# Kernel optimization log

Hardware: AMD Instinct MI355X
Metric: run time of the kernel (lower is better)

Reference implementation:

```python
import jax, jax.numpy as jnp
import numpy as np

N = 50000          # nodes
E = 800000         # edges per metapath
P = 4              # metapaths
IN = 256           # in_size
D = 32 * 8         # out_size * layer_num_heads = 256
SEM_H = 128        # SemanticAttention hidden


def setup_inputs() -> dict:
    key = jax.random.key(0)
    ks = jax.random.split(key, 8)
    h = jax.random.normal(ks[0], (N, IN), dtype=jnp.float32)
    src = jax.random.randint(ks[1], (P, E), 0, N, dtype=jnp.int32)
    dst = jax.random.randint(ks[2], (P, E), 0, N, dtype=jnp.int32)
    # per-metapath GraphConv weights (Glorot-ish scale)
    W_gc = jax.random.normal(ks[3], (P, IN, D), dtype=jnp.float32) / np.sqrt(IN)
    b_gc = jnp.zeros((P, D), dtype=jnp.float32)
    # SemanticAttention: Linear(D, SEM_H) -> tanh -> Linear(SEM_H, 1, bias=False)
    W1 = jax.random.normal(ks[4], (D, SEM_H), dtype=jnp.float32) / np.sqrt(D)
    b1 = jnp.zeros((SEM_H,), dtype=jnp.float32)
    w2 = jax.random.normal(ks[5], (SEM_H,), dtype=jnp.float32) / np.sqrt(SEM_H)
    return {"h": h, "src": src, "dst": dst, "W_gc": W_gc, "b_gc": b_gc,
            "W1": W1, "b1": b1, "w2": w2}


def _graph_conv(h, src, dst, W, b):
    # DGL GraphConv with norm='both': D_dst^{-1/2} A D_src^{-1/2} (h W) + b
    ones = jnp.ones((src.shape[0],), dtype=h.dtype)
    deg_out = jnp.clip(jax.ops.segment_sum(ones, src, num_segments=N), 1.0)
    deg_in = jnp.clip(jax.ops.segment_sum(ones, dst, num_segments=N), 1.0)
    x = (h @ W) * jax.lax.rsqrt(deg_out)[:, None]          # [N, D]
    agg = jax.ops.segment_sum(x[src], dst, num_segments=N)  # gather-scatter [N, D]
    return agg * jax.lax.rsqrt(deg_in)[:, None] + b


def reference(h, src, dst, W_gc, b_gc, W1, b1, w2):
    # per-metapath GraphConv (fixed small loop over P metapaths)
    zs = [_graph_conv(h, src[p], dst[p], W_gc[p], b_gc[p]) for p in range(P)]
    z = jnp.stack(zs, axis=1)                               # [N, P, D]
    # SemanticAttention: project -> mean over nodes -> softmax over metapaths
    s = jnp.tanh(z @ W1 + b1) @ w2                          # [N, P]
    beta = jax.nn.softmax(s.mean(axis=0), axis=0)           # [P]
    return jnp.einsum('npd,p->nd', z, beta)                 # [N, D]
```

## Files before the change

### kernel.cpp

```cpp
#include <hip/hip_runtime.h>

#define NN 50000
#define NE 800000
#define NP 4
#define DIN 256
#define DD 256
#define NH 128
#define SA 40
#define NSEG 16
#define SEGE (NE / NSEG)
#define FCH 8192
#define NFC 7
#define SPAD(k) ((k) + ((k) >> 5))

typedef __attribute__((ext_vector_type(8))) short bf16x8;
typedef __attribute__((ext_vector_type(4))) float f32x4;

__device__ __forceinline__ unsigned short f2bf(float f) {
  unsigned u = __float_as_uint(f);
  u += 0x7fff + ((u >> 16) & 1);
  return (unsigned short)(u >> 16);
}
__device__ __forceinline__ float bfl(unsigned u) { return __uint_as_float(u << 16); }
__device__ __forceinline__ float bfh(unsigned u) { return __uint_as_float(u & 0xffff0000u); }


__global__ __launch_bounds__(256) void hist2d_kernel(const int* __restrict__ idx,
                                                     int* __restrict__ cnt) {
  int bx = blockIdx.x;
  int c = bx % NFC, s = bx / NFC;
  int p = blockIdx.y;
  int base = c * FCH, nk = min(FCH, NN - base);
  __shared__ int hs[FCH];
  for (int k = threadIdx.x; k < FCH; k += 256) hs[k] = 0;
  __syncthreads();
  const int4* a4 = (const int4*)(idx + (size_t)p * NE + (size_t)s * SEGE);
  for (int i = threadIdx.x; i < SEGE / 4; i += 256) {
    int4 v = a4[i];
    int k;
    k = v.x - base; if ((unsigned)k < (unsigned)nk) atomicAdd(&hs[k], 1);
    k = v.y - base; if ((unsigned)k < (unsigned)nk) atomicAdd(&hs[k], 1);
    k = v.z - base; if ((unsigned)k < (unsigned)nk) atomicAdd(&hs[k], 1);
    k = v.w - base; if ((unsigned)k < (unsigned)nk) atomicAdd(&hs[k], 1);
  }
  __syncthreads();
  int* out = cnt + (size_t)(p * NSEG + s) * NN + base;
  for (int k = threadIdx.x; k < nk; k += 256) out[k] = hs[k];
}


__global__ __launch_bounds__(1024) void scanA_kernel(
    int* __restrict__ cntD, const int* __restrict__ cntS,
    float* __restrict__ rin, float* __restrict__ rout,
    int* __restrict__ row_ptr, int* __restrict__ chunkdeg) {
  int c = blockIdx.x, p = blockIdx.y;
  int base = c * FCH, nk = min(FCH, NN - base);
  __shared__ int sdeg[FCH + (FCH >> 5)];
  __shared__ int wtot[16], wexc[16];
  int t = threadIdx.x;
  for (int kk = t; kk < FCH; kk += 1024) {
    int run = 0;
    if (kk < nk) {
      size_t o = (size_t)(p * NSEG) * NN + base + kk;
      for (int s = 0; s < NSEG; ++s) {
        size_t oo = o + (size_t)s * NN;
        int v = cntD[oo];
        cntD[oo] = run;
        run += v;
      }
      rin[(size_t)p * NN + base + kk] = rsqrtf((float)max(run, 1));
      int rs = 0;
      for (int s = 0; s < NSEG; ++s) rs += cntS[o + (size_t)s * NN];
      rout[(size_t)p * NN + base + kk] = rsqrtf((float)max(rs, 1));
    }
    sdeg[SPAD(kk)] = run;
  }
  __syncthreads();
  int loc[8];
  int ssum = 0;
#pragma unroll
  for (int j = 0; j < 8; ++j) { loc[j] = ssum; ssum += sdeg[SPAD(t * 8 + j)]; }
  int incl = ssum;
  int lane = t & 63, w = t >> 6;
#pragma unroll
  for (int o = 1; o < 64; o <<= 1) {
    int v = __shfl_up(incl, o);
    if (lane >= o) incl += v;
  }
  if (lane == 63) wtot[w] = incl;
  __syncthreads();
  if (t == 0) {
    int r = 0;
    for (int i = 0; i < 16; ++i) { wexc[i] = r; r += wtot[i]; }
  }
  __syncthreads();
  int tbase = wexc[w] + incl - ssum;
  int* rp = row_ptr + (size_t)p * (NN + 1) + base;
#pragma unroll
  for (int j = 0; j < 8; ++j) {
    int k = t * 8 + j;
    if (k < nk) rp[k] = tbase + loc[j];
  }
  if (t == 1023) chunkdeg[p * NFC + c] = tbase + ssum;
}


__global__ void scanB_kernel(const int* __restrict__ chunkdeg, int* __restrict__ chunk_base,
                             int* __restrict__ row_ptr) {
  int t = threadIdx.x;
  if (t < NP) {
    int run = 0;
    for (int c = 0; c < NFC; ++c) { chunk_base[t * NFC + c] = run; run += chunkdeg[t * NFC + c]; }
    row_ptr[(size_t)t * (NN + 1) + NN] = NE;
  }
}

__global__ __launch_bounds__(1024) void rpfin_kernel(int* __restrict__ row_ptr,
                                                     const int* __restrict__ chunk_base) {
  int k = blockIdx.x * 1024 + threadIdx.x, p = blockIdx.y;
  if (k < NN) row_ptr[(size_t)p * (NN + 1) + k] += chunk_base[p * NFC + (k >> 13)];
}


__global__ __launch_bounds__(256) void scatter_kernel(
    const int* __restrict__ src, const int* __restrict__ dst,
    const int* __restrict__ cntD, const int* __restrict__ row_ptr, int* __restrict__ col) {
  int bx = blockIdx.x;
  int c = bx % NFC, s = bx / NFC;
  int p = blockIdx.y;
  int base = c * FCH, nk = min(FCH, NN - base);
  __shared__ int cur[FCH];
  for (int k = threadIdx.x; k < nk; k += 256)
    cur[k] = row_ptr[(size_t)p * (NN + 1) + base + k] +
             cntD[(size_t)(p * NSEG + s) * NN + base + k];
  __syncthreads();
  const int4* d4 = (const int4*)(dst + (size_t)p * NE + (size_t)s * SEGE);
  const int4* s4 = (const int4*)(src + (size_t)p * NE + (size_t)s * SEGE);
  int* colp = col + (size_t)p * NE;
  for (int i = threadIdx.x; i < SEGE / 4; i += 256) {
    int4 dv = d4[i];
    int4 sv = s4[i];
    int k;
    k = dv.x - base; if ((unsigned)k < (unsigned)nk) colp[atomicAdd(&cur[k], 1)] = sv.x;
    k = dv.y - base; if ((unsigned)k < (unsigned)nk) colp[atomicAdd(&cur[k], 1)] = sv.y;
    k = dv.z - base; if ((unsigned)k < (unsigned)nk) colp[atomicAdd(&cur[k], 1)] = sv.z;
    k = dv.w - base; if ((unsigned)k < (unsigned)nk) colp[atomicAdd(&cur[k], 1)] = sv.w;
  }
}


__global__ void cvt_h_kernel(const float4* __restrict__ h4, ushort4* __restrict__ h2) {
  int i = blockIdx.x * blockDim.x + threadIdx.x;
  if (i >= NN * DIN / 4) return;
  float4 v = h4[i];
  ushort4 o;
  o.x = f2bf(v.x); o.y = f2bf(v.y); o.z = f2bf(v.z); o.w = f2bf(v.w);
  h2[i] = o;
}


__global__ __launch_bounds__(256) void agg_kernel(
    const ushort* __restrict__ h2, const int* __restrict__ col,
    const int* __restrict__ row_ptr, const float* __restrict__ rout,
    const float* __restrict__ rin, ushort* __restrict__ g) {
  int p = blockIdx.y;
  int v = blockIdx.x * 4 + (threadIdx.x >> 6);
  int lane = threadIdx.x & 63;
  const int* colp = col + (size_t)p * NE;
  const float* rop = rout + (size_t)p * NN;
  int beg = row_ptr[p * (NN + 1) + v], end = row_ptr[p * (NN + 1) + v + 1];
  const uint2* hv = (const uint2*)h2;
  float a0 = 0, a1 = 0, a2 = 0, a3 = 0, b0 = 0, b1 = 0, b2 = 0, b3 = 0;
  int j = beg;
  for (; j + 1 < end; j += 2) {
    int s0 = colp[j], s1 = colp[j + 1];
    float r0 = rop[s0], r1 = rop[s1];
    uint2 u0 = hv[(size_t)s0 * 64 + lane];
    uint2 u1 = hv[(size_t)s1 * 64 + lane];
    a0 = fmaf(r0, bfl(u0.x), a0); a1 = fmaf(r0, bfh(u0.x), a1);
    a2 = fmaf(r0, bfl(u0.y), a2); a3 = fmaf(r0, bfh(u0.y), a3);
    b0 = fmaf(r1, bfl(u1.x), b0); b1 = fmaf(r1, bfh(u1.x), b1);
    b2 = fmaf(r1, bfl(u1.y), b2); b3 = fmaf(r1, bfh(u1.y), b3);
  }
  if (j < end) {
    int s0 = colp[j];
    float r0 = rop[s0];
    uint2 u0 = hv[(size_t)s0 * 64 + lane];
    a0 = fmaf(r0, bfl(u0.x), a0); a1 = fmaf(r0, bfh(u0.x), a1);
    a2 = fmaf(r0, bfl(u0.y), a2); a3 = fmaf(r0, bfh(u0.y), a3);
  }
  float ri = rin[(size_t)p * NN + v];
  ushort4 o;
  o.x = f2bf((a0 + b0) * ri); o.y = f2bf((a1 + b1) * ri);
  o.z = f2bf((a2 + b2) * ri); o.w = f2bf((a3 + b3) * ri);
  ((ushort4*)(g + ((size_t)p * NN + v) * DIN))[lane] = o;
}


__global__ void wmul_kernel(const float* __restrict__ Wgc, const float* __restrict__ W1,
                            ushort* __restrict__ Mt) {
  int p = blockIdx.y, k = blockIdx.x, j = threadIdx.x;
  const float* wrow = Wgc + ((size_t)p * DIN + k) * DD;
  float s = 0.f;
  for (int d = 0; d < DD; ++d) s = fmaf(wrow[d], W1[(size_t)d * NH + j], s);
  Mt[((size_t)p * NH + j) * DIN + k] = f2bf(s);
}

__global__ void cvec_kernel(const float* __restrict__ bgc, const float* __restrict__ W1,
                            const float* __restrict__ b1, float* __restrict__ cvec) {
  int p = blockIdx.x, j = threadIdx.x;
  const float* b = bgc + (size_t)p * DD;
  float s = b1[j];
  for (int d = 0; d < DD; ++d) s = fmaf(b[d], W1[(size_t)d * NH + j], s);
  cvec[p * NH + j] = s;
}


__global__ __launch_bounds__(256) void gemm_sem(
    const ushort* __restrict__ g, const ushort* __restrict__ Mt,
    const float* __restrict__ cvec, const float* __restrict__ w2,
    float* __restrict__ ssum) {
  __shared__ ushort As[128 * SA];
  __shared__ ushort Bs[128 * SA];
  __shared__ float wsumf[4];
  const int tid = threadIdx.x;
  const int p = blockIdx.y;
  const int row0 = blockIdx.x * 128;
  const int wave = tid >> 6, lane = tid & 63;
  const int wr = wave >> 1, wc = wave & 1;
  const int srow = tid >> 2, sseg = tid & 3;
  const int fr = lane & 15, fk = (lane >> 4) * 8;
  const ushort* Ag = g + (size_t)p * NN * DIN;
  const ushort* Bg = Mt + (size_t)p * NH * DIN;
  int ar0 = row0 + srow; if (ar0 >= NN) ar0 = NN - 1;
  int ar1 = row0 + srow + 64; if (ar1 >= NN) ar1 = NN - 1;
  f32x4 acc[4][4] = {};
  for (int k2 = 0; k2 < DIN; k2 += 32) {
    uint4 av0 = *(const uint4*)(Ag + (size_t)ar0 * DIN + k2 + sseg * 8);
    uint4 av1 = *(const uint4*)(Ag + (size_t)ar1 * DIN + k2 + sseg * 8);
    uint4 bv0 = *(const uint4*)(Bg + (size_t)srow * DIN + k2 + sseg * 8);
    uint4 bv1 = *(const uint4*)(Bg + (size_t)(srow + 64) * DIN + k2 + sseg * 8);
    __syncthreads();
    *(uint4*)&As[srow * SA + sseg * 8] = av0;
    *(uint4*)&As[(srow + 64) * SA + sseg * 8] = av1;
    *(uint4*)&Bs[srow * SA + sseg * 8] = bv0;
    *(uint4*)&Bs[(srow + 64) * SA + sseg * 8] = bv1;
    __syncthreads();
    bf16x8 af[4], bfv[4];
#pragma unroll
    for (int t = 0; t < 4; ++t) {
      af[t] = *(const bf16x8*)&As[(wr * 64 + t * 16 + fr) * SA + fk];
      bfv[t] = *(const bf16x8*)&Bs[(wc * 64 + t * 16 + fr) * SA + fk];
    }
#pragma unroll
    for (int mt = 0; mt < 4; ++mt)
#pragma unroll
      for (int nt = 0; nt < 4; ++nt)
        acc[mt][nt] = __builtin_amdgcn_mfma_f32_16x16x32_bf16(af[mt], bfv[nt], acc[mt][nt], 0, 0, 0);
  }
  float s = 0.f;
#pragma unroll
  for (int nt = 0; nt < 4; ++nt) {
    int c = wc * 64 + nt * 16 + fr;
    float cc = cvec[p * NH + c];
    float ww = w2[c];
#pragma unroll
    for (int mt = 0; mt < 4; ++mt)
#pragma unroll
      for (int i = 0; i < 4; ++i) {
        int r = row0 + wr * 64 + mt * 16 + (lane >> 4) * 4 + i;
        if (r < NN) {
          float x = acc[mt][nt][i] + cc;
          x = fminf(fmaxf(x, -15.f), 15.f);
          float e = __expf(2.f * x);
          s = fmaf((e - 1.f) / (e + 1.f), ww, s);
        }
      }
  }
#pragma unroll
  for (int o = 32; o > 0; o >>= 1) s += __shfl_down(s, o);
  if (lane == 0) wsumf[wave] = s;
  __syncthreads();
  if (tid == 0) atomicAdd(&ssum[p], wsumf[0] + wsumf[1] + wsumf[2] + wsumf[3]);
}


__global__ void beta_kernel(const float* __restrict__ ssum, const float* __restrict__ bgc,
                            float* __restrict__ beta, float* __restrict__ bout) {
  __shared__ float sb[NP];
  if (threadIdx.x == 0) {
    float m[NP];
    float mx = -1e30f;
    for (int p = 0; p < NP; ++p) {
      m[p] = ssum[p] / (float)NN;
      mx = fmaxf(mx, m[p]);
    }
    float tot = 0.f;
    for (int p = 0; p < NP; ++p) { m[p] = expf(m[p] - mx); tot += m[p]; }
    for (int p = 0; p < NP; ++p) { sb[p] = m[p] / tot; beta[p] = sb[p]; }
  }
  __syncthreads();
  int d = threadIdx.x;
  float s = 0.f;
  for (int p = 0; p < NP; ++p) s = fmaf(sb[p], bgc[p * DD + d], s);
  bout[d] = s;
}

__global__ void scaleWt_kernel(const float* __restrict__ Wgc, const float* __restrict__ beta,
                               ushort* __restrict__ Wt) {
  int i = blockIdx.x * blockDim.x + threadIdx.x;
  if (i >= DD * NP * DIN) return;
  int n = i >> 10;
  int pk = i & 1023;
  int p = pk >> 8, k = pk & 255;
  Wt[i] = f2bf(beta[p] * Wgc[((size_t)p * DIN + k) * DD + n]);
}


__global__ __launch_bounds__(256) void gemm_main(
    const ushort* __restrict__ g, const ushort* __restrict__ Wt,
    const float* __restrict__ bout, float* __restrict__ out) {
  __shared__ ushort As[128 * SA];
  __shared__ ushort Bs[128 * SA];
  const int tid = threadIdx.x;
  const int row0 = blockIdx.x * 128;
  const int col0 = blockIdx.y * 128;
  const int wave = tid >> 6, lane = tid & 63;
  const int wr = wave >> 1, wc = wave & 1;
  const int srow = tid >> 2, sseg = tid & 3;
  const int fr = lane & 15, fk = (lane >> 4) * 8;
  int ar0 = row0 + srow; if (ar0 >= NN) ar0 = NN - 1;
  int ar1 = row0 + srow + 64; if (ar1 >= NN) ar1 = NN - 1;
  f32x4 acc[4][4] = {};
  for (int p = 0; p < NP; ++p) {
    const ushort* Ag = g + (size_t)p * NN * DIN;
    for (int k2 = 0; k2 < DIN; k2 += 32) {
      uint4 av0 = *(const uint4*)(Ag + (size_t)ar0 * DIN + k2 + sseg * 8);
      uint4 av1 = *(const uint4*)(Ag + (size_t)ar1 * DIN + k2 + sseg * 8);
      uint4 bv0 = *(const uint4*)(Wt + (size_t)(col0 + srow) * (NP * DIN) + p * DIN + k2 + sseg * 8);
      uint4 bv1 = *(const uint4*)(Wt + (size_t)(col0 + srow + 64) * (NP * DIN) + p * DIN + k2 + sseg * 8);
      __syncthreads();
      *(uint4*)&As[srow * SA + sseg * 8] = av0;
      *(uint4*)&As[(srow + 64) * SA + sseg * 8] = av1;
      *(uint4*)&Bs[srow * SA + sseg * 8] = bv0;
      *(uint4*)&Bs[(srow + 64) * SA + sseg * 8] = bv1;
      __syncthreads();
      bf16x8 af[4], bfv[4];
#pragma unroll
      for (int t = 0; t < 4; ++t) {
        af[t] = *(const bf16x8*)&As[(wr * 64 + t * 16 + fr) * SA + fk];
        bfv[t] = *(const bf16x8*)&Bs[(wc * 64 + t * 16 + fr) * SA + fk];
      }
#pragma unroll
      for (int mt = 0; mt < 4; ++mt)
#pragma unroll
        for (int nt = 0; nt < 4; ++nt)
          acc[mt][nt] = __builtin_amdgcn_mfma_f32_16x16x32_bf16(af[mt], bfv[nt], acc[mt][nt], 0, 0, 0);
    }
  }
#pragma unroll
  for (int nt = 0; nt < 4; ++nt) {
    int c = col0 + wc * 64 + nt * 16 + fr;
    float bb = bout[c];
#pragma unroll
    for (int mt = 0; mt < 4; ++mt)
#pragma unroll
      for (int i = 0; i < 4; ++i) {
        int r = row0 + wr * 64 + mt * 16 + (lane >> 4) * 4 + i;
        if (r < NN) out[(size_t)r * DD + c] = acc[mt][nt][i] + bb;
      }
  }
}


extern "C" void kernel_launch(void* const* d_in, const int* in_sizes, int n_in,
                              void* d_out, int out_size, void* d_ws, size_t ws_size,
                              hipStream_t stream) {
  const float* h = (const float*)d_in[0];
  const int* src = (const int*)d_in[1];
  const int* dst = (const int*)d_in[2];
  const float* Wgc = (const float*)d_in[3];
  const float* bgc = (const float*)d_in[4];
  const float* W1 = (const float*)d_in[5];
  const float* b1 = (const float*)d_in[6];
  const float* w2 = (const float*)d_in[7];
  float* out = (float*)d_out;

  char* base = (char*)d_ws;
  size_t off = 0;
  auto alloc = [&](size_t bytes) -> char* {
    char* ptr = base + off;
    off = (off + bytes + 255) & ~(size_t)255;
    return ptr;
  };
  int* cntD = (int*)alloc((size_t)NP * NSEG * NN * sizeof(int));
  int* cntS = (int*)alloc((size_t)NP * NSEG * NN * sizeof(int));
  float* rin = (float*)alloc((size_t)NP * NN * sizeof(float));
  float* rout = (float*)alloc((size_t)NP * NN * sizeof(float));
  int* row_ptr = (int*)alloc((size_t)NP * (NN + 1) * sizeof(int));
  int* chunkdeg = (int*)alloc((size_t)NP * NFC * sizeof(int));
  int* chunk_base = (int*)alloc((size_t)NP * NFC * sizeof(int));
  ushort* h2 = (ushort*)alloc((size_t)NN * DIN * sizeof(ushort));
  ushort* g = (ushort*)alloc((size_t)NP * NN * DIN * sizeof(ushort));
  ushort* Mt = (ushort*)alloc((size_t)NP * NH * DIN * sizeof(ushort));
  ushort* Wt = (ushort*)alloc((size_t)DD * NP * DIN * sizeof(ushort));
  float* cvec = (float*)alloc((size_t)NP * NH * sizeof(float));
  float* ssum = (float*)alloc(NP * sizeof(float));
  float* beta = (float*)alloc(NP * sizeof(float));
  float* bout = (float*)alloc(DD * sizeof(float));
  int* colbuf = (int*)cntS;
  if (off > ws_size) return;

  hipMemsetAsync(ssum, 0, NP * sizeof(float), stream);

  hist2d_kernel<<<dim3(NFC * NSEG, NP), 256, 0, stream>>>(dst, cntD);
  hist2d_kernel<<<dim3(NFC * NSEG, NP), 256, 0, stream>>>(src, cntS);
  scanA_kernel<<<dim3(NFC, NP), 1024, 0, stream>>>(cntD, cntS, rin, rout, row_ptr, chunkdeg);
  scanB_kernel<<<1, 64, 0, stream>>>(chunkdeg, chunk_base, row_ptr);
  rpfin_kernel<<<dim3((NN + 1023) / 1024, NP), 1024, 0, stream>>>(row_ptr, chunk_base);
  cvt_h_kernel<<<(NN * DIN / 4 + 255) / 256, 256, 0, stream>>>((const float4*)h, (ushort4*)h2);
  scatter_kernel<<<dim3(NFC * NSEG, NP), 256, 0, stream>>>(src, dst, cntD, row_ptr, colbuf);
  agg_kernel<<<dim3(NN / 4, NP), 256, 0, stream>>>(h2, colbuf, row_ptr, rout, rin, g);
  wmul_kernel<<<dim3(DIN, NP), NH, 0, stream>>>(Wgc, W1, Mt);
  cvec_kernel<<<NP, NH, 0, stream>>>(bgc, W1, b1, cvec);
  gemm_sem<<<dim3((NN + 127) / 128, NP), 256, 0, stream>>>(g, Mt, cvec, w2, ssum);
  beta_kernel<<<1, 256, 0, stream>>>(ssum, bgc, beta, bout);
  scaleWt_kernel<<<(DD * NP * DIN + 255) / 256, 256, 0, stream>>>(Wgc, beta, Wt);
  gemm_main<<<dim3((NN + 127) / 128, 2), 256, 0, stream>>>(g, Wt, bout, out);
}
```

Before: 656.9 us.

## Fuse histograms, merge weight kernels, widen main GEMM tile, add nontemporal hints

Merges the src and dst degree histograms into one kernel so each edge segment is read in a single pass. Folds the bias-vector kernel into the weight-product kernel as one extra block. Widens the final GEMM to cover all 256 output columns per 512-thread block, so each row of g is loaded once instead of twice. Adds nontemporal load and store hints to the streaming buffers (edge lists, h, g, col, out) to reduce cache pollution, at some risk of losing reuse where data is read again later.

Result: slower. 737.3 us (+12.2%).

```diff
diff --git a/kernel.cpp b/kernel.cpp
--- a/kernel.cpp
+++ b/kernel.cpp
@@ -15,6 +15,9 @@
 
 typedef __attribute__((ext_vector_type(8))) short bf16x8;
 typedef __attribute__((ext_vector_type(4))) float f32x4;
+typedef __attribute__((ext_vector_type(4))) int i32x4;
+typedef __attribute__((ext_vector_type(4))) unsigned u32x4;
+typedef __attribute__((ext_vector_type(4))) unsigned short u16x4;
 
 __device__ __forceinline__ unsigned short f2bf(float f) {
   unsigned u = __float_as_uint(f);
@@ -25,27 +28,39 @@
 __device__ __forceinline__ float bfh(unsigned u) { return __uint_as_float(u & 0xffff0000u); }
 
 
-__global__ __launch_bounds__(256) void hist2d_kernel(const int* __restrict__ idx,
-                                                     int* __restrict__ cnt) {
+__global__ __launch_bounds__(256) void hist2d_both_kernel(
+    const int* __restrict__ src, const int* __restrict__ dst,
+    int* __restrict__ cntS, int* __restrict__ cntD) {
   int bx = blockIdx.x;
   int c = bx % NFC, s = bx / NFC;
   int p = blockIdx.y;
   int base = c * FCH, nk = min(FCH, NN - base);
-  __shared__ int hs[FCH];
-  for (int k = threadIdx.x; k < FCH; k += 256) hs[k] = 0;
-  __syncthreads();
-  const int4* a4 = (const int4*)(idx + (size_t)p * NE + (size_t)s * SEGE);
+  __shared__ int hsS[FCH];
+  __shared__ int hsD[FCH];
+  for (int k = threadIdx.x; k < FCH; k += 256) { hsS[k] = 0; hsD[k] = 0; }
+  __syncthreads();
+  const i32x4* s4 = (const i32x4*)(src + (size_t)p * NE + (size_t)s * SEGE);
+  const i32x4* d4 = (const i32x4*)(dst + (size_t)p * NE + (size_t)s * SEGE);
   for (int i = threadIdx.x; i < SEGE / 4; i += 256) {
-    int4 v = a4[i];
+    i32x4 sv = __builtin_nontemporal_load(&s4[i]);
+    i32x4 dv = __builtin_nontemporal_load(&d4[i]);
     int k;
-    k = v.x - base; if ((unsigned)k < (unsigned)nk) atomicAdd(&hs[k], 1);
-    k = v.y - base; if ((unsigned)k < (unsigned)nk) atomicAdd(&hs[k], 1);
-    k = v.z - base; if ((unsigned)k < (unsigned)nk) atomicAdd(&hs[k], 1);
-    k = v.w - base; if ((unsigned)k < (unsigned)nk) atomicAdd(&hs[k], 1);
-  }
-  __syncthreads();
-  int* out = cnt + (size_t)(p * NSEG + s) * NN + base;
-  for (int k = threadIdx.x; k < nk; k += 256) out[k] = hs[k];
+    k = sv.x - base; if ((unsigned)k < (unsigned)nk) atomicAdd(&hsS[k], 1);
+    k = sv.y - base; if ((unsigned)k < (unsigned)nk) atomicAdd(&hsS[k], 1);
+    k = sv.z - base; if ((unsigned)k < (unsigned)nk) atomicAdd(&hsS[k], 1);
+    k = sv.w - base; if ((unsigned)k < (unsigned)nk) atomicAdd(&hsS[k], 1);
+    k = dv.x - base; if ((unsigned)k < (unsigned)nk) atomicAdd(&hsD[k], 1);
+    k = dv.y - base; if ((unsigned)k < (unsigned)nk) atomicAdd(&hsD[k], 1);
+    k = dv.z - base; if ((unsigned)k < (unsigned)nk) atomicAdd(&hsD[k], 1);
+    k = dv.w - base; if ((unsigned)k < (unsigned)nk) atomicAdd(&hsD[k], 1);
+  }
+  __syncthreads();
+  int* oS = cntS + (size_t)(p * NSEG + s) * NN + base;
+  int* oD = cntD + (size_t)(p * NSEG + s) * NN + base;
+  for (int k = threadIdx.x; k < nk; k += 256) {
+    __builtin_nontemporal_store(hsS[k], &oS[k]);
+    __builtin_nontemporal_store(hsD[k], &oD[k]);
+  }
 }
 
 
@@ -131,15 +146,15 @@
   int base = c * FCH, nk = min(FCH, NN - base);
   __shared__ int cur[FCH];
   for (int k = threadIdx.x; k < nk; k += 256)
-    cur[k] = row_ptr[(size_t)p * (NN + 1) + base + k] +
-             cntD[(size_t)(p * NSEG + s) * NN + base + k];
-  __syncthreads();
-  const int4* d4 = (const int4*)(dst + (size_t)p * NE + (size_t)s * SEGE);
-  const int4* s4 = (const int4*)(src + (size_t)p * NE + (size_t)s * SEGE);
+    cur[k] = __builtin_nontemporal_load(&row_ptr[(size_t)p * (NN + 1) + base + k]) +
+             __builtin_nontemporal_load(&cntD[(size_t)(p * NSEG + s) * NN + base + k]);
+  __syncthreads();
+  const i32x4* d4 = (const i32x4*)(dst + (size_t)p * NE + (size_t)s * SEGE);
+  const i32x4* s4 = (const i32x4*)(src + (size_t)p * NE + (size_t)s * SEGE);
   int* colp = col + (size_t)p * NE;
   for (int i = threadIdx.x; i < SEGE / 4; i += 256) {
-    int4 dv = d4[i];
-    int4 sv = s4[i];
+    i32x4 dv = __builtin_nontemporal_load(&d4[i]);
+    i32x4 sv = __builtin_nontemporal_load(&s4[i]);
     int k;
     k = dv.x - base; if ((unsigned)k < (unsigned)nk) colp[atomicAdd(&cur[k], 1)] = sv.x;
     k = dv.y - base; if ((unsigned)k < (unsigned)nk) colp[atomicAdd(&cur[k], 1)] = sv.y;
@@ -149,11 +164,11 @@
 }
 
 
-__global__ void cvt_h_kernel(const float4* __restrict__ h4, ushort4* __restrict__ h2) {
+__global__ void cvt_h_kernel(const f32x4* __restrict__ h4, u16x4* __restrict__ h2) {
   int i = blockIdx.x * blockDim.x + threadIdx.x;
   if (i >= NN * DIN / 4) return;
-  float4 v = h4[i];
-  ushort4 o;
+  f32x4 v = __builtin_nontemporal_load(&h4[i]);
+  u16x4 o;
   o.x = f2bf(v.x); o.y = f2bf(v.y); o.z = f2bf(v.z); o.w = f2bf(v.w);
   h2[i] = o;
 }
@@ -173,7 +188,8 @@
   float a0 = 0, a1 = 0, a2 = 0, a3 = 0, b0 = 0, b1 = 0, b2 = 0, b3 = 0;
   int j = beg;
   for (; j + 1 < end; j += 2) {
-    int s0 = colp[j], s1 = colp[j + 1];
+    int s0 = __builtin_nontemporal_load(&colp[j]);
+    int s1 = __builtin_nontemporal_load(&colp[j + 1]);
     float r0 = rop[s0], r1 = rop[s1];
     uint2 u0 = hv[(size_t)s0 * 64 + lane];
     uint2 u1 = hv[(size_t)s1 * 64 + lane];
@@ -183,36 +199,35 @@
     b2 = fmaf(r1, bfl(u1.y), b2); b3 = fmaf(r1, bfh(u1.y), b3);
   }
   if (j < end) {
-    int s0 = colp[j];
+    int s0 = __builtin_nontemporal_load(&colp[j]);
     float r0 = rop[s0];
     uint2 u0 = hv[(size_t)s0 * 64 + lane];
     a0 = fmaf(r0, bfl(u0.x), a0); a1 = fmaf(r0, bfh(u0.x), a1);
     a2 = fmaf(r0, bfl(u0.y), a2); a3 = fmaf(r0, bfh(u0.y), a3);
   }
   float ri = rin[(size_t)p * NN + v];
-  ushort4 o;
+  u16x4 o;
   o.x = f2bf((a0 + b0) * ri); o.y = f2bf((a1 + b1) * ri);
   o.z = f2bf((a2 + b2) * ri); o.w = f2bf((a3 + b3) * ri);
-  ((ushort4*)(g + ((size_t)p * NN + v) * DIN))[lane] = o;
-}
-
-
-__global__ void wmul_kernel(const float* __restrict__ Wgc, const float* __restrict__ W1,
-                            ushort* __restrict__ Mt) {
+  __builtin_nontemporal_store(o, &((u16x4*)(g + ((size_t)p * NN + v) * DIN))[lane]);
+}
+
+
+__global__ void wmulc_kernel(const float* __restrict__ Wgc, const float* __restrict__ W1,
+                             const float* __restrict__ bgc, const float* __restrict__ b1,
+                             ushort* __restrict__ Mt, float* __restrict__ cvec) {
   int p = blockIdx.y, k = blockIdx.x, j = threadIdx.x;
-  const float* wrow = Wgc + ((size_t)p * DIN + k) * DD;
-  float s = 0.f;
-  for (int d = 0; d < DD; ++d) s = fmaf(wrow[d], W1[(size_t)d * NH + j], s);
-  Mt[((size_t)p * NH + j) * DIN + k] = f2bf(s);
-}
-
-__global__ void cvec_kernel(const float* __restrict__ bgc, const float* __restrict__ W1,
-                            const float* __restrict__ b1, float* __restrict__ cvec) {
-  int p = blockIdx.x, j = threadIdx.x;
-  const float* b = bgc + (size_t)p * DD;
-  float s = b1[j];
-  for (int d = 0; d < DD; ++d) s = fmaf(b[d], W1[(size_t)d * NH + j], s);
-  cvec[p * NH + j] = s;
+  if (k < DIN) {
+    const float* wrow = Wgc + ((size_t)p * DIN + k) * DD;
+    float s = 0.f;
+    for (int d = 0; d < DD; ++d) s = fmaf(wrow[d], W1[(size_t)d * NH + j], s);
+    Mt[((size_t)p * NH + j) * DIN + k] = f2bf(s);
+  } else {
+    const float* b = bgc + (size_t)p * DD;
+    float s = b1[j];
+    for (int d = 0; d < DD; ++d) s = fmaf(b[d], W1[(size_t)d * NH + j], s);
+    cvec[p * NH + j] = s;
+  }
 }
 
 
@@ -236,15 +251,15 @@
   int ar1 = row0 + srow + 64; if (ar1 >= NN) ar1 = NN - 1;
   f32x4 acc[4][4] = {};
   for (int k2 = 0; k2 < DIN; k2 += 32) {
-    uint4 av0 = *(const uint4*)(Ag + (size_t)ar0 * DIN + k2 + sseg * 8);
-    uint4 av1 = *(const uint4*)(Ag + (size_t)ar1 * DIN + k2 + sseg * 8);
-    uint4 bv0 = *(const uint4*)(Bg + (size_t)srow * DIN + k2 + sseg * 8);
-    uint4 bv1 = *(const uint4*)(Bg + (size_t)(srow + 64) * DIN + k2 + sseg * 8);
+    u32x4 av0 = __builtin_nontemporal_load((const u32x4*)(Ag + (size_t)ar0 * DIN + k2 + sseg * 8));
+    u32x4 av1 = __builtin_nontemporal_load((const u32x4*)(Ag + (size_t)ar1 * DIN + k2 + sseg * 8));
+    u32x4 bv0 = *(const u32x4*)(Bg + (size_t)srow * DIN + k2 + sseg * 8);
+    u32x4 bv1 = *(const u32x4*)(Bg + (size_t)(srow + 64) * DIN + k2 + sseg * 8);
     __syncthreads();
-    *(uint4*)&As[srow * SA + sseg * 8] = av0;
-    *(uint4*)&As[(srow + 64) * SA + sseg * 8] = av1;
-    *(uint4*)&Bs[srow * SA + sseg * 8] = bv0;
-    *(uint4*)&Bs[(srow + 64) * SA + sseg * 8] = bv1;
+    *(u32x4*)&As[srow * SA + sseg * 8] = av0;
+    *(u32x4*)&As[(srow + 64) * SA + sseg * 8] = av1;
+    *(u32x4*)&Bs[srow * SA + sseg * 8] = bv0;
+    *(u32x4*)&Bs[(srow + 64) * SA + sseg * 8] = bv1;
     __syncthreads();
     bf16x8 af[4], bfv[4];
 #pragma unroll
@@ -317,33 +332,29 @@
 }
 
 
-__global__ __launch_bounds__(256) void gemm_main(
+__global__ __launch_bounds__(512) void gemm_main(
     const ushort* __restrict__ g, const ushort* __restrict__ Wt,
     const float* __restrict__ bout, float* __restrict__ out) {
   __shared__ ushort As[128 * SA];
-  __shared__ ushort Bs[128 * SA];
+  __shared__ ushort Bs[256 * SA];
   const int tid = threadIdx.x;
   const int row0 = blockIdx.x * 128;
-  const int col0 = blockIdx.y * 128;
   const int wave = tid >> 6, lane = tid & 63;
-  const int wr = wave >> 1, wc = wave & 1;
+  const int wr = wave >> 2, wc = wave & 3;
   const int srow = tid >> 2, sseg = tid & 3;
   const int fr = lane & 15, fk = (lane >> 4) * 8;
   int ar0 = row0 + srow; if (ar0 >= NN) ar0 = NN - 1;
-  int ar1 = row0 + srow + 64; if (ar1 >= NN) ar1 = NN - 1;
   f32x4 acc[4][4] = {};
   for (int p = 0; p < NP; ++p) {
     const ushort* Ag = g + (size_t)p * NN * DIN;
     for (int k2 = 0; k2 < DIN; k2 += 32) {
-      uint4 av0 = *(const uint4*)(Ag + (size_t)ar0 * DIN + k2 + sseg * 8);
-      uint4 av1 = *(const uint4*)(Ag + (size_t)ar1 * DIN + k2 + sseg * 8);
-      uint4 bv0 = *(const uint4*)(Wt + (size_t)(col0 + srow) * (NP * DIN) + p * DIN + k2 + sseg * 8);
-      uint4 bv1 = *(const uint4*)(Wt + (size_t)(col0 + srow + 64) * (NP * DIN) + p * DIN + k2 + sseg * 8);
+      u32x4 av0 = __builtin_nontemporal_load((const u32x4*)(Ag + (size_t)ar0 * DIN + k2 + sseg * 8));
+      u32x4 bv0 = *(const u32x4*)(Wt + (size_t)srow * (NP * DIN) + p * DIN + k2 + sseg * 8);
+      u32x4 bv1 = *(const u32x4*)(Wt + (size_t)(srow + 128) * (NP * DIN) + p * DIN + k2 + sseg * 8);
       __syncthreads();
-      *(uint4*)&As[srow * SA + sseg * 8] = av0;
-      *(uint4*)&As[(srow + 64) * SA + sseg * 8] = av1;
-      *(uint4*)&Bs[srow * SA + sseg * 8] = bv0;
-      *(uint4*)&Bs[(srow + 64) * SA + sseg * 8] = bv1;
+      *(u32x4*)&As[srow * SA + sseg * 8] = av0;
+      *(u32x4*)&Bs[srow * SA + sseg * 8] = bv0;
+      *(u32x4*)&Bs[(srow + 128) * SA + sseg * 8] = bv1;
       __syncthreads();
       bf16x8 af[4], bfv[4];
 #pragma unroll
@@ -360,14 +371,14 @@
   }
 #pragma unroll
   for (int nt = 0; nt < 4; ++nt) {
-    int c = col0 + wc * 64 + nt * 16 + fr;
+    int c = wc * 64 + nt * 16 + fr;
     float bb = bout[c];
 #pragma unroll
     for (int mt = 0; mt < 4; ++mt)
 #pragma unroll
       for (int i = 0; i < 4; ++i) {
         int r = row0 + wr * 64 + mt * 16 + (lane >> 4) * 4 + i;
-        if (r < NN) out[(size_t)r * DD + c] = acc[mt][nt][i] + bb;
+        if (r < NN) __builtin_nontemporal_store(acc[mt][nt][i] + bb, &out[(size_t)r * DD + c]);
       }
   }
 }
@@ -411,20 +422,18 @@
   int* colbuf = (int*)cntS;
   if (off > ws_size) return;
 
-  hipMemsetAsync(ssum, 0, NP * sizeof(float), stream);
-
-  hist2d_kernel<<<dim3(NFC * NSEG, NP), 256, 0, stream>>>(dst, cntD);
-  hist2d_kernel<<<dim3(NFC * NSEG, NP), 256, 0, stream>>>(src, cntS);
+  (void)hipMemsetAsync(ssum, 0, NP * sizeof(float), stream);
+
+  hist2d_both_kernel<<<dim3(NFC * NSEG, NP), 256, 0, stream>>>(src, dst, cntS, cntD);
   scanA_kernel<<<dim3(NFC, NP), 1024, 0, stream>>>(cntD, cntS, rin, rout, row_ptr, chunkdeg);
   scanB_kernel<<<1, 64, 0, stream>>>(chunkdeg, chunk_base, row_ptr);
   rpfin_kernel<<<dim3((NN + 1023) / 1024, NP), 1024, 0, stream>>>(row_ptr, chunk_base);
-  cvt_h_kernel<<<(NN * DIN / 4 + 255) / 256, 256, 0, stream>>>((const float4*)h, (ushort4*)h2);
+  cvt_h_kernel<<<(NN * DIN / 4 + 255) / 256, 256, 0, stream>>>((const f32x4*)h, (u16x4*)h2);
   scatter_kernel<<<dim3(NFC * NSEG, NP), 256, 0, stream>>>(src, dst, cntD, row_ptr, colbuf);
   agg_kernel<<<dim3(NN / 4, NP), 256, 0, stream>>>(h2, colbuf, row_ptr, rout, rin, g);
-  wmul_kernel<<<dim3(DIN, NP), NH, 0, stream>>>(Wgc, W1, Mt);
-  cvec_kernel<<<NP, NH, 0, stream>>>(bgc, W1, b1, cvec);
+  wmulc_kernel<<<dim3(DIN + 1, NP), NH, 0, stream>>>(Wgc, W1, bgc, b1, Mt, cvec);
   gemm_sem<<<dim3((NN + 127) / 128, NP), 256, 0, stream>>>(g, Mt, cvec, w2, ssum);
   beta_kernel<<<1, 256, 0, stream>>>(ssum, bgc, beta, bout);
   scaleWt_kernel<<<(DD * NP * DIN + 255) / 256, 256, 0, stream>>>(Wgc, beta, Wt);
-  gemm_main<<<dim3((NN + 127) / 128, 2), 256, 0, stream>>>(g, Wt, bout, out);
-}
+  gemm_main<<<(NN + 127) / 128, 512, 0, stream>>>(g, Wt, bout, out);
+}
```
